# Optimization experiments

Hardware: AMD Instinct MI355X
Metric: run time of the kernel (lower is better)

## Reference

```python
import jax, jax.numpy as jnp
import numpy as np

B, T, C, H = 2, 2048, 1024, 16
D = C // H


def setup_inputs() -> dict:
    key = jax.random.key(0)
    k1, k2, k3 = jax.random.split(key, 3)
    x = jax.random.normal(k1, (B, T, C), dtype=jnp.float32)
    w_attn = jax.random.normal(k2, (3 * C, C), dtype=jnp.float32) * (1.0 / np.sqrt(C))
    w_proj = jax.random.normal(k3, (C, C), dtype=jnp.float32) * (1.0 / np.sqrt(C))
    # causal mask, 1 = keep, 0 = masked (matches att.masked_fill(mask == 0, -inf))
    mask = jnp.tril(jnp.ones((T, T), dtype=jnp.int32))[None, None, :, :]
    return {"x": x, "w_attn": w_attn, "w_proj": w_proj, "mask": mask}


def reference(x, w_attn, w_proj, mask):
    Bq, Tq, Cq = x.shape
    qkv = x @ w_attn.T                      # [B,T,3C] (torch Linear: x @ W^T)
    q, k, v = jnp.split(qkv, 3, axis=2)
    # [B,T,C] -> [B,H,T,D]
    q = q.reshape(Bq, Tq, H, D).transpose(0, 2, 1, 3)
    k = k.reshape(Bq, Tq, H, D).transpose(0, 2, 1, 3)
    v = v.reshape(Bq, Tq, H, D).transpose(0, 2, 1, 3)
    att = jnp.einsum("bhqd,bhkd->bhqk", q, k) * (1.0 / np.sqrt(D))
    att = jnp.where(mask == 0, -jnp.inf, att)
    att = jax.nn.softmax(att, axis=-1)      # dropout p=0.0 -> identity
    y = jnp.einsum("bhqk,bhkd->bhqd", att, v)
    y = y.transpose(0, 2, 1, 3).reshape(Bq, Tq, Cq)
    return y @ w_proj.T
```

## Files before the change

kernel.cpp:

```cpp
#include <hip/hip_runtime.h>
#include <hip/hip_bf16.h>
#include <math.h>


typedef __attribute__((ext_vector_type(4))) float floatx4;
typedef __attribute__((ext_vector_type(8))) __bf16 bf16x8;
typedef __attribute__((ext_vector_type(4))) __bf16 bf16x4;

#define MFMA_BF16(a, b, c) __builtin_amdgcn_mfma_f32_16x16x32_bf16((a), (b), (c), 0, 0, 0)

typedef __attribute__((address_space(1))) const uint32_t* gas_t;
typedef __attribute__((address_space(3))) uint32_t* las_t;
__device__ inline void gl2lds16(const void* g, void* l) {
    __builtin_amdgcn_global_load_lds((gas_t)g, (las_t)l, 16, 0, 0);
}

__device__ inline uint4 cvt8_f32_bf16(const float4 a, const float4 b) {
    union { __hip_bfloat16 h[8]; uint4 u; } c;
    c.h[0] = __float2bfloat16(a.x); c.h[1] = __float2bfloat16(a.y);
    c.h[2] = __float2bfloat16(a.z); c.h[3] = __float2bfloat16(a.w);
    c.h[4] = __float2bfloat16(b.x); c.h[5] = __float2bfloat16(b.y);
    c.h[6] = __float2bfloat16(b.z); c.h[7] = __float2bfloat16(b.w);
    return c.u;
}

__global__ __launch_bounds__(256) void cvt_all(
    const float* __restrict__ x, const float* __restrict__ wa,
    const float* __restrict__ wp, __hip_bfloat16* __restrict__ out)
{
    const size_t e = ((size_t)blockIdx.x * 256 + threadIdx.x) * 8;
    const float* src; size_t off;
    if (e < 4194304)      { src = x;  off = e; }
    else if (e < 7340032) { src = wa; off = e - 4194304; }
    else                  { src = wp; off = e - 7340032; }
    const float4 a = *(const float4*)&src[off];
    const float4 b = *(const float4*)&src[off + 4];
    *(uint4*)&out[e] = cvt8_f32_bf16(a, b);
}

__global__ __launch_bounds__(256) void gemm_qkv(
    const __hip_bfloat16* __restrict__ A,
    const __hip_bfloat16* __restrict__ Bt,
    __hip_bfloat16* __restrict__ qk,
    __hip_bfloat16* __restrict__ vt, int K)
{
    __shared__ __hip_bfloat16 As0[128][32];
    __shared__ __hip_bfloat16 As1[128][32];
    __shared__ __hip_bfloat16 Bs0[128][32];
    __shared__ __hip_bfloat16 Bs1[128][32];

    const int tid  = threadIdx.x;
    const int wave = tid >> 6;
    const int lane = tid & 63;
    const int quad = lane >> 4;
    const int l15  = lane & 15;
    const int wrow = wave >> 1;
    const int wcol = wave & 1;
    const int bm = blockIdx.y * 128;
    const int bn = blockIdx.x * 128;

    floatx4 acc[4][4];
#pragma unroll
    for (int i = 0; i < 4; ++i)
#pragma unroll
        for (int j = 0; j < 4; ++j)
            acc[i][j] = (floatx4){0.f, 0.f, 0.f, 0.f};

    const int srow = lane >> 2;
    const int scol = (lane & 3) * 8;

    const __hip_bfloat16* Abase = A  + (size_t)bm * K;
    const __hip_bfloat16* Bbase = Bt + (size_t)bn * K;

    for (int k0 = 0; k0 < K; k0 += 64) {
#pragma unroll
        for (int c = 0; c < 2; ++c) {
            const int rbase = wave * 32 + c * 16;
            const size_t ga = (size_t)(rbase + srow) * K + k0 + scol;
            gl2lds16(&Abase[ga],      &As0[rbase][0]);
            gl2lds16(&Abase[ga + 32], &As1[rbase][0]);
            gl2lds16(&Bbase[ga],      &Bs0[rbase][0]);
            gl2lds16(&Bbase[ga + 32], &Bs1[rbase][0]);
        }
        __syncthreads();

#pragma unroll
        for (int kd = 0; kd < 2; ++kd) {
            const __hip_bfloat16 (*Ap)[32] = kd ? As1 : As0;
            const __hip_bfloat16 (*Bp)[32] = kd ? Bs1 : Bs0;
            bf16x8 af[4], bfv[4];
#pragma unroll
            for (int i = 0; i < 4; ++i)
                af[i] = *(const bf16x8*)&Ap[wrow * 64 + i * 16 + l15][quad * 8];
#pragma unroll
            for (int j = 0; j < 4; ++j)
                bfv[j] = *(const bf16x8*)&Bp[wcol * 64 + j * 16 + l15][quad * 8];
#pragma unroll
            for (int i = 0; i < 4; ++i)
#pragma unroll
                for (int j = 0; j < 4; ++j)
                    acc[i][j] = MFMA_BF16(af[i], bfv[j], acc[i][j]);
        }
        __syncthreads();
    }

    if (bn < 2048) {
        const float sc = (bn < 1024) ? 0.18033688f : 1.0f;
#pragma unroll
        for (int i = 0; i < 4; ++i)
#pragma unroll
            for (int j = 0; j < 4; ++j)
#pragma unroll
                for (int r = 0; r < 4; ++r) {
                    const int row = bm + wrow * 64 + i * 16 + quad * 4 + r;
                    const int col = bn + wcol * 64 + j * 16 + l15;
                    qk[(size_t)row * 2048 + col] = __float2bfloat16(acc[i][j][r] * sc);
                }
    } else {
#pragma unroll
        for (int i = 0; i < 4; ++i)
#pragma unroll
            for (int j = 0; j < 4; ++j) {
                const int trow0 = bm + wrow * 64 + i * 16 + quad * 4;
                const int d = bn - 2048 + wcol * 64 + j * 16 + l15;
                const int b = trow0 >> 11, t0 = trow0 & 2047;
                union { __hip_bfloat16 h[4]; uint2 u; } pk;
#pragma unroll
                for (int r = 0; r < 4; ++r) pk.h[r] = __float2bfloat16(acc[i][j][r]);
                *(uint2*)&vt[((size_t)(b * 16 + (d >> 6)) * 64 + (d & 63)) * 2048 + t0] = pk.u;
            }
    }
}

__global__ __launch_bounds__(256) void gemm_bt_mfma_n64(
    const __hip_bfloat16* __restrict__ A,
    const __hip_bfloat16* __restrict__ Bt,
    float* __restrict__ C, int M, int N, int K)
{
    __shared__ __hip_bfloat16 As[128][32];
    __shared__ __hip_bfloat16 Bs[64][32];

    const int tid  = threadIdx.x;
    const int wave = tid >> 6;
    const int lane = tid & 63;
    const int quad = lane >> 4;
    const int l15  = lane & 15;
    const int wrow = wave >> 1;
    const int wcol = wave & 1;
    const int bm = blockIdx.y * 128;
    const int bn = blockIdx.x * 64;

    floatx4 acc[4][2];
#pragma unroll
    for (int i = 0; i < 4; ++i)
#pragma unroll
        for (int j = 0; j < 2; ++j)
            acc[i][j] = (floatx4){0.f, 0.f, 0.f, 0.f};

    const int srow = lane >> 2;
    const int scol = (lane & 3) * 8;

    const __hip_bfloat16* Abase = A  + (size_t)bm * K;
    const __hip_bfloat16* Bbase = Bt + (size_t)bn * K;

    for (int k0 = 0; k0 < K; k0 += 32) {
        {
            const int ra0 = wave * 32;
            gl2lds16(&Abase[(size_t)(ra0 + srow) * K + k0 + scol], &As[ra0][0]);
            gl2lds16(&Abase[(size_t)(ra0 + 16 + srow) * K + k0 + scol], &As[ra0 + 16][0]);
            const int rb0 = wave * 16;
            gl2lds16(&Bbase[(size_t)(rb0 + srow) * K + k0 + scol], &Bs[rb0][0]);
        }
        __syncthreads();

        bf16x8 af[4], bfv[2];
#pragma unroll
        for (int i = 0; i < 4; ++i)
            af[i] = *(const bf16x8*)&As[wrow * 64 + i * 16 + l15][quad * 8];
#pragma unroll
        for (int j = 0; j < 2; ++j)
            bfv[j] = *(const bf16x8*)&Bs[wcol * 32 + j * 16 + l15][quad * 8];

#pragma unroll
        for (int i = 0; i < 4; ++i)
#pragma unroll
            for (int j = 0; j < 2; ++j)
                acc[i][j] = MFMA_BF16(af[i], bfv[j], acc[i][j]);
        __syncthreads();
    }

#pragma unroll
    for (int i = 0; i < 4; ++i)
#pragma unroll
        for (int j = 0; j < 2; ++j)
#pragma unroll
            for (int r = 0; r < 4; ++r) {
                const int row = bm + wrow * 64 + i * 16 + quad * 4 + r;
                const int col = bn + wcol * 32 + j * 16 + l15;
                C[(size_t)row * N + col] = acc[i][j][r];
            }
}

__global__ __launch_bounds__(256) void attn_kernel(
    const __hip_bfloat16* __restrict__ qk,
    const __hip_bfloat16* __restrict__ vt,
    float* __restrict__ part)
{
    constexpr int T = 2048;
    __shared__ __hip_bfloat16 Ks[64][72];
    __shared__ __hip_bfloat16 Vt[64][72];

    const int bh = blockIdx.x;
    const int b = bh >> 4, h = bh & 15;
    const int p = blockIdx.y;
    const int s = blockIdx.z;
    const int q0A = p * 64;
    const int q0B = (31 - p) * 64;

    const int tid  = threadIdx.x;
    const int wave = tid >> 6;
    const int lane = tid & 63;
    const int quad = lane >> 4;
    const int l15  = lane & 15;

    const __hip_bfloat16* base  = qk + (size_t)b * T * 2048;
    const __hip_bfloat16* vbase = vt + (size_t)((b * 16 + h) * 64) * 2048;

    bf16x8 aqA[2], aqB[2];
#pragma unroll
    for (int kd = 0; kd < 2; ++kd) {
        aqA[kd] = *(const bf16x8*)&base[(size_t)(q0A + wave * 16 + l15) * 2048 + h * 64 + kd * 32 + quad * 8];
        aqB[kd] = *(const bf16x8*)&base[(size_t)(q0B + wave * 16 + l15) * 2048 + h * 64 + kd * 32 + quad * 8];
    }

    bf16x8 ones;
#pragma unroll
    for (int i = 0; i < 8; ++i) ones[i] = (__bf16)1.0f;
    const bf16x4 zero4 = {};

    floatx4 accA[4], accB[4], lTA, lTB;
#pragma unroll
    for (int r = 0; r < 4; ++r) {
        accA[r] = (floatx4){0.f, 0.f, 0.f, 0.f};
        accB[r] = (floatx4){0.f, 0.f, 0.f, 0.f};
    }
    lTA = (floatx4){0.f, 0.f, 0.f, 0.f};
    lTB = (floatx4){0.f, 0.f, 0.f, 0.f};

    const int sr = tid >> 2;
    const int sc = (tid & 3) * 16;
    const int myq = wave * 16 + l15;

    for (int j0 = s * 64; j0 <= q0B; j0 += 128) {
        const bool actA = (j0 <= q0A);
        const bool dgA  = (j0 == q0A);
        const bool dgB  = (j0 == q0B);

        {
            const size_t kg = (size_t)(j0 + sr) * 2048 + 1024 + h * 64 + sc;
            *(uint4*)&Ks[sr][sc]     = *(const uint4*)&base[kg];
            *(uint4*)&Ks[sr][sc + 8] = *(const uint4*)&base[kg + 8];
            const size_t vg = (size_t)sr * 2048 + j0 + sc;
            *(uint4*)&Vt[sr][sc]     = *(const uint4*)&vbase[vg];
            *(uint4*)&Vt[sr][sc + 8] = *(const uint4*)&vbase[vg + 8];
        }
        __syncthreads();

        floatx4 sA[4], sB[4];
#pragma unroll
        for (int jt = 0; jt < 4; ++jt) {
            sA[jt] = (floatx4){0.f, 0.f, 0.f, 0.f};
            sB[jt] = (floatx4){0.f, 0.f, 0.f, 0.f};
        }
#pragma unroll
        for (int jt = 0; jt < 4; ++jt)
#pragma unroll
            for (int kd = 0; kd < 2; ++kd) {
                bf16x8 ak = *(const bf16x8*)&Ks[jt * 16 + l15][kd * 32 + quad * 8];
                sB[jt] = MFMA_BF16(ak, aqB[kd], sB[jt]);
                if (actA) sA[jt] = MFMA_BF16(ak, aqA[kd], sA[jt]);
            }

        bf16x8 pfA[4], pfB[4];
#pragma unroll
        for (int jt = 0; jt < 4; ++jt) {
            const int kvl = jt * 16 + quad * 4;
            bf16x4 lo;
#pragma unroll
            for (int r = 0; r < 4; ++r) {
                float pv = __builtin_amdgcn_exp2f(sB[jt][r]);
                if (dgB && (kvl + r) > myq) pv = 0.f;
                lo[r] = (__bf16)__float2bfloat16(pv);
            }
            pfB[jt] = __builtin_shufflevector(lo, zero4, 0, 1, 2, 3, 4, 5, 6, 7);
            if (actA) {
#pragma unroll
                for (int r = 0; r < 4; ++r) {
                    float pv = __builtin_amdgcn_exp2f(sA[jt][r]);
                    if (dgA && (kvl + r) > myq) pv = 0.f;
                    lo[r] = (__bf16)__float2bfloat16(pv);
                }
                pfA[jt] = __builtin_shufflevector(lo, zero4, 0, 1, 2, 3, 4, 5, 6, 7);
            }
        }

#pragma unroll
        for (int jt = 0; jt < 4; ++jt) {
            lTB = MFMA_BF16(ones, pfB[jt], lTB);
            if (actA) lTA = MFMA_BF16(ones, pfA[jt], lTA);
        }

#pragma unroll
        for (int jd = 0; jd < 4; ++jd)
#pragma unroll
            for (int jt = 0; jt < 4; ++jt) {
                const bf16x4 vlo = *(const bf16x4*)&Vt[jd * 16 + l15][jt * 16 + quad * 4];
                const bf16x8 av = __builtin_shufflevector(vlo, zero4, 0, 1, 2, 3, 4, 5, 6, 7);
                accB[jd] = MFMA_BF16(av, pfB[jt], accB[jd]);
                if (actA) accA[jd] = MFMA_BF16(av, pfA[jt], accA[jd]);
            }
        __syncthreads();
    }

    float* pA = part + (size_t)((s * 32 + bh) * 32 + p) * 4160;
    float* pB = part + (size_t)((s * 32 + bh) * 32 + (31 - p)) * 4160;
#pragma unroll
    for (int jd = 0; jd < 4; ++jd)
#pragma unroll
        for (int r = 0; r < 4; ++r) {
            const int d = jd * 16 + quad * 4 + r;
            pA[d * 64 + myq] = accA[jd][r];
            pB[d * 64 + myq] = accB[jd][r];
        }
    if (quad == 0) {
        pA[4096 + myq] = lTA[0];
        pB[4096 + myq] = lTB[0];
    }
}

__global__ __launch_bounds__(256) void combine_kernel(
    const float* __restrict__ part, __hip_bfloat16* __restrict__ y)
{
    const int bh = blockIdx.x, t = blockIdx.y;
    const int b = bh >> 4, h = bh & 15;
    const float* p0 = part + (size_t)((0 * 32 + bh) * 32 + t) * 4160;
    const float* p1 = part + (size_t)((1 * 32 + bh) * 32 + t) * 4160;

    __shared__ float Ls[64][65];
    __shared__ float linv[64];
    const int tid = threadIdx.x;
    if (tid < 64) linv[tid] = 1.f / (p0[4096 + tid] + p1[4096 + tid]);

    const int dr = tid >> 2;
    const int q0 = (tid & 3) * 16;
#pragma unroll
    for (int c = 0; c < 4; ++c) {
        const float4 a = *(const float4*)&p0[dr * 64 + q0 + c * 4];
        const float4 e = *(const float4*)&p1[dr * 64 + q0 + c * 4];
        Ls[dr][q0 + c * 4 + 0] = a.x + e.x;
        Ls[dr][q0 + c * 4 + 1] = a.y + e.y;
        Ls[dr][q0 + c * 4 + 2] = a.z + e.z;
        Ls[dr][q0 + c * 4 + 3] = a.w + e.w;
    }
    __syncthreads();

    const int q  = tid >> 2;
    const int d0 = (tid & 3) * 16;
    const float inv = linv[q];
    union { __hip_bfloat16 hh[16]; uint4 u[2]; } ob;
#pragma unroll
    for (int j = 0; j < 16; ++j)
        ob.hh[j] = __float2bfloat16(Ls[d0 + j][q] * inv);
    __hip_bfloat16* yp = &y[((size_t)(b * 2048 + t * 64 + q)) * 1024 + h * 64 + d0];
    *(uint4*)(yp)     = ob.u[0];
    *(uint4*)(yp + 8) = ob.u[1];
}

extern "C" void kernel_launch(void* const* d_in, const int* in_sizes, int n_in,
                              void* d_out, int out_size, void* d_ws, size_t ws_size,
                              hipStream_t stream)
{
    const float* x      = (const float*)d_in[0];
    const float* w_attn = (const float*)d_in[1];
    const float* w_proj = (const float*)d_in[2];

    float* out = (float*)d_out;
    __hip_bfloat16* xb  = (__hip_bfloat16*)d_ws;
    __hip_bfloat16* wab = xb  + (size_t)4096 * 1024;
    __hip_bfloat16* wpb = wab + (size_t)3072 * 1024;
    __hip_bfloat16* qkb = wpb + (size_t)1024 * 1024;
    __hip_bfloat16* y   = qkb + (size_t)4096 * 2048;
    __hip_bfloat16* vt  = y   + (size_t)4096 * 1024;
    float*          prt = (float*)(vt + (size_t)2048 * 2048);

    cvt_all<<<4096, 256, 0, stream>>>(x, w_attn, w_proj, xb);

    gemm_qkv<<<dim3(24, 32), 256, 0, stream>>>(xb, wab, qkb, vt, 1024);

    attn_kernel<<<dim3(32, 16, 2), 256, 0, stream>>>(qkb, vt, prt);
    combine_kernel<<<dim3(32, 32), 256, 0, stream>>>(prt, y);

    gemm_bt_mfma_n64<<<dim3(16, 32), 256, 0, stream>>>(y, wpb, out, 4096, 1024, 1024);
}
```

Baseline: 212.7 us.

## Double-buffer K/V tiles in attention and use half-width bf16 MFMA for PV

Adds a two-stage LDS ring for K and V tiles. The next tile's global loads are issued into registers before the current tile's MFMAs and written to the other buffer afterwards, which removes one barrier per iteration and overlaps load latency with compute. Separately, the P·V and row-sum products now use the 16x16x16 bf16 MFMA on 4-element operands instead of zero-padding to the 16x16x32 form, halving the wasted MFMA work. The cost is doubled LDS use and extra prefetch registers, which may lower occupancy.

```diff
diff --git a/kernel.cpp b/kernel.cpp
--- a/kernel.cpp
+++ b/kernel.cpp
@@ -6,8 +6,23 @@
 typedef __attribute__((ext_vector_type(4))) float floatx4;
 typedef __attribute__((ext_vector_type(8))) __bf16 bf16x8;
 typedef __attribute__((ext_vector_type(4))) __bf16 bf16x4;
+typedef __attribute__((ext_vector_type(4))) short short4v;
 
 #define MFMA_BF16(a, b, c) __builtin_amdgcn_mfma_f32_16x16x32_bf16((a), (b), (c), 0, 0, 0)
+
+#if __has_builtin(__builtin_amdgcn_mfma_f32_16x16x16bf16_1k)
+__device__ inline floatx4 mfma16(bf16x4 a, bf16x4 b, floatx4 c) {
+    union { bf16x4 h; short4v s; } ua, ub;
+    ua.h = a; ub.h = b;
+    return __builtin_amdgcn_mfma_f32_16x16x16bf16_1k(ua.s, ub.s, c, 0, 0, 0);
+}
+#else
+__device__ inline floatx4 mfma16(bf16x4 a, bf16x4 b, floatx4 c) {
+    const bf16x4 z = {};
+    return MFMA_BF16(__builtin_shufflevector(a, z, 0, 1, 2, 3, 4, 5, 6, 7),
+                     __builtin_shufflevector(b, z, 0, 1, 2, 3, 4, 5, 6, 7), c);
+}
+#endif
 
 typedef __attribute__((address_space(1))) const uint32_t* gas_t;
 typedef __attribute__((address_space(3))) uint32_t* las_t;
@@ -207,8 +222,8 @@
     float* __restrict__ part)
 {
     constexpr int T = 2048;
-    __shared__ __hip_bfloat16 Ks[64][72];
-    __shared__ __hip_bfloat16 Vt[64][72];
+    __shared__ __hip_bfloat16 Ks[2][64][72];
+    __shared__ __hip_bfloat16 Vt[2][64][72];
 
     const int bh = blockIdx.x;
     const int b = bh >> 4, h = bh & 15;
@@ -233,10 +248,9 @@
         aqB[kd] = *(const bf16x8*)&base[(size_t)(q0B + wave * 16 + l15) * 2048 + h * 64 + kd * 32 + quad * 8];
     }
 
-    bf16x8 ones;
-#pragma unroll
-    for (int i = 0; i < 8; ++i) ones[i] = (__bf16)1.0f;
-    const bf16x4 zero4 = {};
+    bf16x4 ones4;
+#pragma unroll
+    for (int i = 0; i < 4; ++i) ones4[i] = (__bf16)1.0f;
 
     floatx4 accA[4], accB[4], lTA, lTB;
 #pragma unroll
@@ -251,20 +265,33 @@
     const int sc = (tid & 3) * 16;
     const int myq = wave * 16 + l15;
 
+    {
+        const int j0 = s * 64;
+        const size_t kg = (size_t)(j0 + sr) * 2048 + 1024 + h * 64 + sc;
+        *(uint4*)&Ks[0][sr][sc]     = *(const uint4*)&base[kg];
+        *(uint4*)&Ks[0][sr][sc + 8] = *(const uint4*)&base[kg + 8];
+        const size_t vg = (size_t)sr * 2048 + j0 + sc;
+        *(uint4*)&Vt[0][sr][sc]     = *(const uint4*)&vbase[vg];
+        *(uint4*)&Vt[0][sr][sc + 8] = *(const uint4*)&vbase[vg + 8];
+    }
+    __syncthreads();
+
+    int cur = 0;
     for (int j0 = s * 64; j0 <= q0B; j0 += 128) {
-        const bool actA = (j0 <= q0A);
-        const bool dgA  = (j0 == q0A);
-        const bool dgB  = (j0 == q0B);
-
-        {
-            const size_t kg = (size_t)(j0 + sr) * 2048 + 1024 + h * 64 + sc;
-            *(uint4*)&Ks[sr][sc]     = *(const uint4*)&base[kg];
-            *(uint4*)&Ks[sr][sc + 8] = *(const uint4*)&base[kg + 8];
-            const size_t vg = (size_t)sr * 2048 + j0 + sc;
-            *(uint4*)&Vt[sr][sc]     = *(const uint4*)&vbase[vg];
-            *(uint4*)&Vt[sr][sc + 8] = *(const uint4*)&vbase[vg + 8];
-        }
-        __syncthreads();
+        const bool actA  = (j0 <= q0A);
+        const bool dgA   = (j0 == q0A);
+        const bool dgB   = (j0 == q0B);
+        const bool hnext = (j0 + 128 <= q0B);
+
+        uint4 pk0, pk1, pv0, pv1;
+        if (hnext) {
+            const size_t kg = (size_t)(j0 + 128 + sr) * 2048 + 1024 + h * 64 + sc;
+            pk0 = *(const uint4*)&base[kg];
+            pk1 = *(const uint4*)&base[kg + 8];
+            const size_t vg = (size_t)sr * 2048 + (j0 + 128) + sc;
+            pv0 = *(const uint4*)&vbase[vg];
+            pv1 = *(const uint4*)&vbase[vg + 8];
+        }
 
         floatx4 sA[4], sB[4];
 #pragma unroll
@@ -276,50 +303,55 @@
         for (int jt = 0; jt < 4; ++jt)
 #pragma unroll
             for (int kd = 0; kd < 2; ++kd) {
-                bf16x8 ak = *(const bf16x8*)&Ks[jt * 16 + l15][kd * 32 + quad * 8];
+                bf16x8 ak = *(const bf16x8*)&Ks[cur][jt * 16 + l15][kd * 32 + quad * 8];
                 sB[jt] = MFMA_BF16(ak, aqB[kd], sB[jt]);
                 if (actA) sA[jt] = MFMA_BF16(ak, aqA[kd], sA[jt]);
             }
 
-        bf16x8 pfA[4], pfB[4];
+        bf16x4 pfA[4], pfB[4];
 #pragma unroll
         for (int jt = 0; jt < 4; ++jt) {
             const int kvl = jt * 16 + quad * 4;
-            bf16x4 lo;
 #pragma unroll
             for (int r = 0; r < 4; ++r) {
                 float pv = __builtin_amdgcn_exp2f(sB[jt][r]);
                 if (dgB && (kvl + r) > myq) pv = 0.f;
-                lo[r] = (__bf16)__float2bfloat16(pv);
-            }
-            pfB[jt] = __builtin_shufflevector(lo, zero4, 0, 1, 2, 3, 4, 5, 6, 7);
+                pfB[jt][r] = (__bf16)__float2bfloat16(pv);
+            }
             if (actA) {
 #pragma unroll
                 for (int r = 0; r < 4; ++r) {
                     float pv = __builtin_amdgcn_exp2f(sA[jt][r]);
                     if (dgA && (kvl + r) > myq) pv = 0.f;
-                    lo[r] = (__bf16)__float2bfloat16(pv);
+                    pfA[jt][r] = (__bf16)__float2bfloat16(pv);
                 }
-                pfA[jt] = __builtin_shufflevector(lo, zero4, 0, 1, 2, 3, 4, 5, 6, 7);
             }
         }
 
 #pragma unroll
         for (int jt = 0; jt < 4; ++jt) {
-            lTB = MFMA_BF16(ones, pfB[jt], lTB);
-            if (actA) lTA = MFMA_BF16(ones, pfA[jt], lTA);
+            lTB = mfma16(ones4, pfB[jt], lTB);
+            if (actA) lTA = mfma16(ones4, pfA[jt], lTA);
         }
 
 #pragma unroll
         for (int jd = 0; jd < 4; ++jd)
 #pragma unroll
             for (int jt = 0; jt < 4; ++jt) {
-                const bf16x4 vlo = *(const bf16x4*)&Vt[jd * 16 + l15][jt * 16 + quad * 4];
-                const bf16x8 av = __builtin_shufflevector(vlo, zero4, 0, 1, 2, 3, 4, 5, 6, 7);
-                accB[jd] = MFMA_BF16(av, pfB[jt], accB[jd]);
-                if (actA) accA[jd] = MFMA_BF16(av, pfA[jt], accA[jd]);
-            }
-        __syncthreads();
+                const bf16x4 av = *(const bf16x4*)&Vt[cur][jd * 16 + l15][jt * 16 + quad * 4];
+                accB[jd] = mfma16(av, pfB[jt], accB[jd]);
+                if (actA) accA[jd] = mfma16(av, pfA[jt], accA[jd]);
+            }
+
+        if (hnext) {
+            const int nxt = cur ^ 1;
+            *(uint4*)&Ks[nxt][sr][sc]     = pk0;
+            *(uint4*)&Ks[nxt][sr][sc + 8] = pk1;
+            *(uint4*)&Vt[nxt][sr][sc]     = pv0;
+            *(uint4*)&Vt[nxt][sr][sc + 8] = pv1;
+            __syncthreads();
+        }
+        cur ^= 1;
     }
 
     float* pA = part + (size_t)((s * 32 + bh) * 32 + p) * 4160;
```

New measurement: 206.6 us. 2.9% less time.
